# Performance work log

Measured on AMD Instinct MI355X. Metric: run time of the kernel, lower is better.

## Reference

```python
import jax, jax.numpy as jnp
import numpy as np


def _segment_sparsemax(x, batch, B):
    """Per-group sparsemax over a flat ragged tensor.

    x: [N] float values; batch: [N] sorted int group ids in [0, B).
    Groups are contiguous, so an in-group descending sort is a stable
    lexsort on (batch, -x); per-group cumsum is a global cumsum minus the
    cumsum value just before each group's start offset.
    """
    N = x.shape[0]
    num_nodes = jax.ops.segment_sum(jnp.ones(N, jnp.int32), batch, num_segments=B)  # [B]
    start = jnp.concatenate([jnp.zeros(1, jnp.int32), jnp.cumsum(num_nodes)[:-1]])  # [B]

    # shift by per-group max for numerical stability (as in torch forward)
    gmax = jax.ops.segment_max(x, batch, num_segments=B)
    xs = x - gmax[batch]

    # descending sort within each contiguous group
    order = jnp.lexsort((-xs, batch))
    sx = xs[order]  # [N], group-wise descending; group layout unchanged

    # per-group cumulative sum via global cumsum + start offsets
    cs = jnp.cumsum(sx)
    off = jnp.where(start > 0, cs[jnp.maximum(start - 1, 0)], jnp.zeros((), sx.dtype))  # [B]
    seg_cs = cs - off[batch] - 1.0  # input_cumsum - 1.0

    # rho = 1..n_g within each group
    rho = (jnp.arange(N, dtype=jnp.int32) - start[batch] + 1).astype(xs.dtype)

    support = rho * sx > seg_cs  # [N] bool
    supp_size = jax.ops.segment_sum(support.astype(jnp.int32), batch, num_segments=B)  # [B]

    idx = jnp.maximum(supp_size + start - 1, 0)  # [B]
    tau = seg_cs[idx] / supp_size.astype(xs.dtype)  # [B]

    return jnp.maximum(xs - tau[batch], 0.0)


def setup_inputs() -> dict:
    key = jax.random.key(0)
    k1, k2 = jax.random.split(key)
    N = 8_388_608
    B = 4096
    x = jax.random.normal(k1, (N,), dtype=jnp.float32)
    batch = jnp.sort(jax.random.randint(k2, (N,), 0, B)).astype(jnp.int64)
    return {"x": x, "batch": batch, "num_groups": B}


def reference(x, batch, num_groups):
    batch = batch.astype(jnp.int32)
    return _segment_sparsemax(x, batch, int(num_groups))
```

## Files before the change

kernel.cpp:

```cpp
#include <hip/hip_runtime.h>

#define BLK 256
#define QPT 3
#define CAPB (QPT * BLK * 4)
#define CCAP 320


__device__ __forceinline__ float wave_max(float v) {
#pragma unroll
  for (int o = 32; o; o >>= 1) v = fmaxf(v, __shfl_xor(v, o));
  return v;
}
__device__ __forceinline__ float wave_sum(float v) {
#pragma unroll
  for (int o = 32; o; o >>= 1) v += __shfl_xor(v, o);
  return v;
}
__device__ __forceinline__ int wave_sum_i(int v) {
#pragma unroll
  for (int o = 32; o; o >>= 1) v += __shfl_xor(v, o);
  return v;
}

__device__ __forceinline__ void block_sum_cnt(float& s, int& c, float* redf, int* redi, int tid) {
  s = wave_sum(s); c = wave_sum_i(c);
  __syncthreads();
  if ((tid & 63) == 0) { redf[tid >> 6] = s; redi[tid >> 6] = c; }
  __syncthreads();
  s = redf[0] + redf[1] + redf[2] + redf[3];
  c = redi[0] + redi[1] + redi[2] + redi[3];
}


extern "C" __global__ void __launch_bounds__(256)
build_starts(const int* __restrict__ batch, int* __restrict__ starts,
             const int* __restrict__ pB, int N) {
  const int B = *pB;
  const long long tid = (long long)blockIdx.x * 256 + threadIdx.x;
  const long long i0 = tid * 8;
  if (i0 >= N) return;
  int v[8];
  if (i0 + 8 <= N) {
    const int4 a = *(const int4*)(batch + i0);
    const int4 b = *(const int4*)(batch + i0 + 4);
    v[0] = a.x; v[1] = a.y; v[2] = a.z; v[3] = a.w;
    v[4] = b.x; v[5] = b.y; v[6] = b.z; v[7] = b.w;
  } else {
#pragma unroll
    for (int t = 0; t < 8; ++t) v[t] = (i0 + t < N) ? batch[i0 + t] : 0;
  }
  int prev = (i0 == 0) ? -1 : batch[i0 - 1];
#pragma unroll
  for (int t = 0; t < 8; ++t) {
    if (i0 + t >= N) break;
    const int cur = v[t];
    for (int g = prev + 1; g <= cur; ++g) starts[g] = (int)(i0 + t);
    prev = cur;
  }
  if (i0 + 8 >= N) {
    for (int g = prev + 1; g <= B; ++g) starts[g] = N;
  }
}


extern "C" __global__ void __launch_bounds__(BLK)
sparsemax_groups(const float* __restrict__ x, const int* __restrict__ starts,
                 const int* __restrict__ pB, float* __restrict__ out, int N) {
  __shared__ float redf[4];
  __shared__ int   redi[4];
  __shared__ float cand[CCAP];
  __shared__ float sorted[64];
  __shared__ int   s_cnt;
  __shared__ float s_csum;
  __shared__ float s_tau;
  const int tid  = threadIdx.x;
  const int lane = tid & 63;
  const int w    = tid >> 6;
  const int B = *pB;

  for (int g = blockIdx.x; g < B; g += gridDim.x) {
    const int s = starts[g];
    const int e = starts[g + 1];
    const int n = e - s;
    if (n <= 0) continue;
    const int a0 = s & ~3;

    if (e - a0 <= CAPB) {
      float4 r[QPT];
      float lmax = -INFINITY;
#pragma unroll
      for (int j = 0; j < QPT; ++j) {
        const int idx = a0 + (j * BLK + tid) * 4;
        float4 v = make_float4(-INFINITY, -INFINITY, -INFINITY, -INFINITY);
        if (idx < e) {
          if (idx + 4 <= N) {
            v = *(const float4*)(x + idx);
          } else {
            if (idx + 0 < N) v.x = x[idx + 0];
            if (idx + 1 < N) v.y = x[idx + 1];
            if (idx + 2 < N) v.z = x[idx + 2];
            if (idx + 3 < N) v.w = x[idx + 3];
          }
          if (idx + 0 < s || idx + 0 >= e) v.x = -INFINITY;
          if (idx + 1 < s || idx + 1 >= e) v.y = -INFINITY;
          if (idx + 2 < s || idx + 2 >= e) v.z = -INFINITY;
          if (idx + 3 < s || idx + 3 >= e) v.w = -INFINITY;
        }
        r[j] = v;
        lmax = fmaxf(lmax, fmaxf(fmaxf(v.x, v.y), fmaxf(v.z, v.w)));
      }
      lmax = wave_max(lmax);
      if (lane == 0) redf[w] = lmax;
      if (tid == 0) { s_cnt = 0; s_csum = 0.0f; }
      __syncthreads();
      const float gmax = fmaxf(fmaxf(redf[0], redf[1]), fmaxf(redf[2], redf[3]));
      const float thr = gmax - 1.0f;

      float wsum = 0.0f;
#pragma unroll
      for (int j = 0; j < QPT; ++j) {
        const float vv[4] = {r[j].x, r[j].y, r[j].z, r[j].w};
#pragma unroll
        for (int t = 0; t < 4; ++t) {
          const bool p = vv[t] > thr;
          const unsigned long long bal = __ballot(p);
          if (bal) {
            int base = 0;
            if (lane == 0) base = atomicAdd(&s_cnt, __popcll(bal));
            base = __shfl(base, 0);
            if (p) {
              const int off = base + __popcll(bal & ((1ull << lane) - 1ull));
              if (off < CCAP) cand[off] = vv[t];
              wsum += vv[t] - gmax;
            }
          }
        }
      }
      wsum = wave_sum(wsum);
      if (lane == 0) atomicAdd(&s_csum, wsum);
      __syncthreads();
      const int c = s_cnt;

      if (c <= 64) {
        if (w == 0) {
          const float v = (lane < c) ? cand[lane] - gmax : 0.0f;
          int rank = 0;
          for (int q = 0; q < c; ++q) {
            const float t = cand[q] - gmax;
            rank += (t > v) || (t == v && q < lane);
          }
          if (lane < c) sorted[rank] = v;
          const float sv = (lane < c) ? sorted[lane] : 0.0f;
          float cs = sv;
#pragma unroll
          for (int o = 1; o < 64; o <<= 1) {
            const float t2 = __shfl_up(cs, o);
            if (lane >= o) cs += t2;
          }
          const int flag = (lane < c) && (sv * (float)(lane + 1) > cs - 1.0f);
          const unsigned long long bal2 = __ballot(flag);
          const int k = 63 - __clzll(bal2);
          const float csk = __shfl(cs, k);
          if (lane == 0) s_tau = (csk - 1.0f) / (float)(k + 1);
        }
      } else if (c <= CCAP) {
        if (w == 0) {
          float tau = (s_csum - 1.0f) / (float)c;
          int cnt = c;
          for (int it = 0; it < 64; ++it) {
            float s2 = 0.0f; int c2 = 0;
            for (int q = lane; q < c; q += 64) {
              const float vs = cand[q] - gmax;
              if (vs > tau) { s2 += vs; c2++; }
            }
            s2 = wave_sum(s2); c2 = wave_sum_i(c2);
            if (c2 == cnt || c2 == 0) break;
            tau = (s2 - 1.0f) / (float)c2; cnt = c2;
          }
          if (lane == 0) s_tau = tau;
        }
      } else {
        float tau = (s_csum - 1.0f) / (float)c;
        int cnt = c;
        for (int it = 0; it < 64; ++it) {
          float s2 = 0.0f; int c2 = 0;
#pragma unroll
          for (int j = 0; j < QPT; ++j) {
            const float vv[4] = {r[j].x, r[j].y, r[j].z, r[j].w};
#pragma unroll
            for (int t = 0; t < 4; ++t) {
              const float vs = vv[t] - gmax;
              if (vs > tau) { s2 += vs; c2++; }
            }
          }
          block_sum_cnt(s2, c2, redf, redi, tid);
          if (c2 == cnt || c2 == 0) break;
          tau = (s2 - 1.0f) / (float)c2; cnt = c2;
        }
        if (tid == 0) s_tau = tau;
      }
      __syncthreads();
      const float sub = s_tau + gmax;

#pragma unroll
      for (int j = 0; j < QPT; ++j) {
        const int idx = a0 + (j * BLK + tid) * 4;
        if (idx >= e) continue;
        if (idx >= s && idx + 4 <= e) {
          float4 o4;
          o4.x = fmaxf(r[j].x - sub, 0.0f);
          o4.y = fmaxf(r[j].y - sub, 0.0f);
          o4.z = fmaxf(r[j].z - sub, 0.0f);
          o4.w = fmaxf(r[j].w - sub, 0.0f);
          *(float4*)(out + idx) = o4;
        } else {
          const float vv[4] = {r[j].x, r[j].y, r[j].z, r[j].w};
#pragma unroll
          for (int t = 0; t < 4; ++t) {
            const int p2 = idx + t;
            if (p2 >= s && p2 < e) out[p2] = fmaxf(vv[t] - sub, 0.0f);
          }
        }
      }
    } else {
      float gmax = -INFINITY;
      for (int i = s + tid; i < e; i += BLK) gmax = fmaxf(gmax, x[i]);
      gmax = wave_max(gmax);
      if (lane == 0) redf[w] = gmax;
      __syncthreads();
      gmax = fmaxf(fmaxf(redf[0], redf[1]), fmaxf(redf[2], redf[3]));
      float bs = 0.0f; int bc = 0;
      for (int i = s + tid; i < e; i += BLK) {
        const float vs = x[i] - gmax;
        if (vs > -1.0f) { bs += vs; bc++; }
      }
      block_sum_cnt(bs, bc, redf, redi, tid);
      float tau = (bs - 1.0f) / (float)bc;
      int cntS = bc;
      for (int it = 0; it < 64; ++it) {
        float s2 = 0.0f; int c2 = 0;
        for (int i = s + tid; i < e; i += BLK) {
          const float vs = x[i] - gmax;
          if (vs > tau) { s2 += vs; c2++; }
        }
        block_sum_cnt(s2, c2, redf, redi, tid);
        if (c2 == cntS || c2 == 0) break;
        tau = (s2 - 1.0f) / (float)c2; cntS = c2;
      }
      const float sub = tau + gmax;
      for (int i = s + tid; i < e; i += BLK) out[i] = fmaxf(x[i] - sub, 0.0f);
    }
  }
}

extern "C" void kernel_launch(void* const* d_in, const int* in_sizes, int n_in,
                              void* d_out, int out_size, void* d_ws, size_t ws_size,
                              hipStream_t stream) {
  const float* x     = (const float*)d_in[0];
  const int*   batch = (const int*)d_in[1];
  const int*   pB    = (const int*)d_in[2];
  float*       out   = (float*)d_out;
  const int N = in_sizes[0];

  int* starts = (int*)d_ws;

  const int g1 = (N + 2047) / 2048;
  build_starts<<<dim3(g1), dim3(256), 0, stream>>>(batch, starts, pB, N);
  sparsemax_groups<<<dim3(4096), dim3(BLK), 0, stream>>>(x, starts, pB, out, N);
}
```

Measured before the change: 111.7 us.

## Process one group per wavefront instead of one group per block

Each 64-lane wavefront now handles a whole group on its own: registers hold up to 10 float4 per lane, and candidate compaction uses a running wave-local count instead of LDS atomics. All block-level reductions and __syncthreads are replaced by wave shuffles, and each wave gets its own candidate and sort buffers. The grid shrinks to 1024 blocks of 4 waves, so there is still one wave per group. The goal is to remove block barriers and atomics, at the cost of higher register pressure and less parallelism within each group.

```diff
diff --git a/kernel.cpp b/kernel.cpp
--- a/kernel.cpp
+++ b/kernel.cpp
@@ -1,8 +1,8 @@
 #include <hip/hip_runtime.h>
 
 #define BLK 256
-#define QPT 3
-#define CAPB (QPT * BLK * 4)
+#define WPT 10
+#define WCAP (WPT * 64 * 4)
 #define CCAP 320
 
 
@@ -20,15 +20,6 @@
 #pragma unroll
   for (int o = 32; o; o >>= 1) v += __shfl_xor(v, o);
   return v;
-}
-
-__device__ __forceinline__ void block_sum_cnt(float& s, int& c, float* redf, int* redi, int tid) {
-  s = wave_sum(s); c = wave_sum_i(c);
-  __syncthreads();
-  if ((tid & 63) == 0) { redf[tid >> 6] = s; redi[tid >> 6] = c; }
-  __syncthreads();
-  s = redf[0] + redf[1] + redf[2] + redf[3];
-  c = redi[0] + redi[1] + redi[2] + redi[3];
 }
 
 
@@ -66,31 +57,26 @@
 extern "C" __global__ void __launch_bounds__(BLK)
 sparsemax_groups(const float* __restrict__ x, const int* __restrict__ starts,
                  const int* __restrict__ pB, float* __restrict__ out, int N) {
-  __shared__ float redf[4];
-  __shared__ int   redi[4];
-  __shared__ float cand[CCAP];
-  __shared__ float sorted[64];
-  __shared__ int   s_cnt;
-  __shared__ float s_csum;
-  __shared__ float s_tau;
+  __shared__ float cand[4][CCAP];
+  __shared__ float sorted_[4][64];
   const int tid  = threadIdx.x;
   const int lane = tid & 63;
   const int w    = tid >> 6;
   const int B = *pB;
 
-  for (int g = blockIdx.x; g < B; g += gridDim.x) {
+  for (int g = blockIdx.x * 4 + w; g < B; g += gridDim.x * 4) {
     const int s = starts[g];
     const int e = starts[g + 1];
     const int n = e - s;
     if (n <= 0) continue;
     const int a0 = s & ~3;
 
-    if (e - a0 <= CAPB) {
-      float4 r[QPT];
+    if (e - a0 <= WCAP) {
+      float4 r[WPT];
       float lmax = -INFINITY;
 #pragma unroll
-      for (int j = 0; j < QPT; ++j) {
-        const int idx = a0 + (j * BLK + tid) * 4;
+      for (int j = 0; j < WPT; ++j) {
+        const int idx = a0 + (j * 64 + lane) * 4;
         float4 v = make_float4(-INFINITY, -INFINITY, -INFINITY, -INFINITY);
         if (idx < e) {
           if (idx + 4 <= N) {
@@ -109,83 +95,72 @@
         r[j] = v;
         lmax = fmaxf(lmax, fmaxf(fmaxf(v.x, v.y), fmaxf(v.z, v.w)));
       }
-      lmax = wave_max(lmax);
-      if (lane == 0) redf[w] = lmax;
-      if (tid == 0) { s_cnt = 0; s_csum = 0.0f; }
-      __syncthreads();
-      const float gmax = fmaxf(fmaxf(redf[0], redf[1]), fmaxf(redf[2], redf[3]));
+      const float gmax = wave_max(lmax);
       const float thr = gmax - 1.0f;
 
+      int cnt = 0;
       float wsum = 0.0f;
 #pragma unroll
-      for (int j = 0; j < QPT; ++j) {
+      for (int j = 0; j < WPT; ++j) {
         const float vv[4] = {r[j].x, r[j].y, r[j].z, r[j].w};
 #pragma unroll
         for (int t = 0; t < 4; ++t) {
           const bool p = vv[t] > thr;
           const unsigned long long bal = __ballot(p);
           if (bal) {
-            int base = 0;
-            if (lane == 0) base = atomicAdd(&s_cnt, __popcll(bal));
-            base = __shfl(base, 0);
             if (p) {
-              const int off = base + __popcll(bal & ((1ull << lane) - 1ull));
-              if (off < CCAP) cand[off] = vv[t];
+              const int off = cnt + __popcll(bal & ((1ull << lane) - 1ull));
+              if (off < CCAP) cand[w][off] = vv[t];
               wsum += vv[t] - gmax;
             }
+            cnt += __popcll(bal);
           }
         }
       }
       wsum = wave_sum(wsum);
-      if (lane == 0) atomicAdd(&s_csum, wsum);
-      __syncthreads();
-      const int c = s_cnt;
-
+      const int c = cnt;
+
+      float tau;
       if (c <= 64) {
-        if (w == 0) {
-          const float v = (lane < c) ? cand[lane] - gmax : 0.0f;
-          int rank = 0;
-          for (int q = 0; q < c; ++q) {
-            const float t = cand[q] - gmax;
-            rank += (t > v) || (t == v && q < lane);
-          }
-          if (lane < c) sorted[rank] = v;
-          const float sv = (lane < c) ? sorted[lane] : 0.0f;
-          float cs = sv;
-#pragma unroll
-          for (int o = 1; o < 64; o <<= 1) {
-            const float t2 = __shfl_up(cs, o);
-            if (lane >= o) cs += t2;
-          }
-          const int flag = (lane < c) && (sv * (float)(lane + 1) > cs - 1.0f);
-          const unsigned long long bal2 = __ballot(flag);
-          const int k = 63 - __clzll(bal2);
-          const float csk = __shfl(cs, k);
-          if (lane == 0) s_tau = (csk - 1.0f) / (float)(k + 1);
-        }
+        const float v = (lane < c) ? cand[w][lane] - gmax : 0.0f;
+        int rank = 0;
+        for (int q = 0; q < c; ++q) {
+          const float t = cand[w][q] - gmax;
+          rank += (t > v) || (t == v && q < lane);
+        }
+        if (lane < c) sorted_[w][rank] = v;
+        const float sv = (lane < c) ? sorted_[w][lane] : 0.0f;
+        float cs = sv;
+#pragma unroll
+        for (int o = 1; o < 64; o <<= 1) {
+          const float t2 = __shfl_up(cs, o);
+          if (lane >= o) cs += t2;
+        }
+        const int flag = (lane < c) && (sv * (float)(lane + 1) > cs - 1.0f);
+        const unsigned long long bal2 = __ballot(flag);
+        const int k = 63 - __clzll(bal2);
+        const float csk = __shfl(cs, k);
+        tau = (csk - 1.0f) / (float)(k + 1);
       } else if (c <= CCAP) {
-        if (w == 0) {
-          float tau = (s_csum - 1.0f) / (float)c;
-          int cnt = c;
-          for (int it = 0; it < 64; ++it) {
-            float s2 = 0.0f; int c2 = 0;
-            for (int q = lane; q < c; q += 64) {
-              const float vs = cand[q] - gmax;
-              if (vs > tau) { s2 += vs; c2++; }
-            }
-            s2 = wave_sum(s2); c2 = wave_sum_i(c2);
-            if (c2 == cnt || c2 == 0) break;
-            tau = (s2 - 1.0f) / (float)c2; cnt = c2;
-          }
-          if (lane == 0) s_tau = tau;
-        }
-      } else {
-        float tau = (s_csum - 1.0f) / (float)c;
-        int cnt = c;
+        tau = (wsum - 1.0f) / (float)c;
+        int cnt2 = c;
         for (int it = 0; it < 64; ++it) {
           float s2 = 0.0f; int c2 = 0;
-#pragma unroll
-          for (int j = 0; j < QPT; ++j) {
+          for (int q = lane; q < c; q += 64) {
+            const float vs = cand[w][q] - gmax;
+            if (vs > tau) { s2 += vs; c2++; }
+          }
+          s2 = wave_sum(s2); c2 = wave_sum_i(c2);
+          if (c2 == cnt2 || c2 == 0) break;
+          tau = (s2 - 1.0f) / (float)c2; cnt2 = c2;
+        }
+      } else {
+        tau = (wsum - 1.0f) / (float)c;
+        int cnt2 = c;
+        for (int it = 0; it < 64; ++it) {
+          float s2 = 0.0f; int c2 = 0;
+#pragma unroll
+          for (int j = 0; j < WPT; ++j) {
             const float vv[4] = {r[j].x, r[j].y, r[j].z, r[j].w};
 #pragma unroll
             for (int t = 0; t < 4; ++t) {
@@ -193,18 +168,17 @@
               if (vs > tau) { s2 += vs; c2++; }
             }
           }
-          block_sum_cnt(s2, c2, redf, redi, tid);
-          if (c2 == cnt || c2 == 0) break;
-          tau = (s2 - 1.0f) / (float)c2; cnt = c2;
-        }
-        if (tid == 0) s_tau = tau;
-      }
-      __syncthreads();
-      const float sub = s_tau + gmax;
-
-#pragma unroll
-      for (int j = 0; j < QPT; ++j) {
-        const int idx = a0 + (j * BLK + tid) * 4;
+          s2 = wave_sum(s2); c2 = wave_sum_i(c2);
+          if (c2 == cnt2 || c2 == 0) break;
+          tau = (s2 - 1.0f) / (float)c2; cnt2 = c2;
+        }
+      }
+
+      const float sub = tau + gmax;
+
+#pragma unroll
+      for (int j = 0; j < WPT; ++j) {
+        const int idx = a0 + (j * 64 + lane) * 4;
         if (idx >= e) continue;
         if (idx >= s && idx + 4 <= e) {
           float4 o4;
@@ -224,31 +198,28 @@
       }
     } else {
       float gmax = -INFINITY;
-      for (int i = s + tid; i < e; i += BLK) gmax = fmaxf(gmax, x[i]);
+      for (int i = s + lane; i < e; i += 64) gmax = fmaxf(gmax, x[i]);
       gmax = wave_max(gmax);
-      if (lane == 0) redf[w] = gmax;
-      __syncthreads();
-      gmax = fmaxf(fmaxf(redf[0], redf[1]), fmaxf(redf[2], redf[3]));
       float bs = 0.0f; int bc = 0;
-      for (int i = s + tid; i < e; i += BLK) {
+      for (int i = s + lane; i < e; i += 64) {
         const float vs = x[i] - gmax;
         if (vs > -1.0f) { bs += vs; bc++; }
       }
-      block_sum_cnt(bs, bc, redf, redi, tid);
+      bs = wave_sum(bs); bc = wave_sum_i(bc);
       float tau = (bs - 1.0f) / (float)bc;
       int cntS = bc;
       for (int it = 0; it < 64; ++it) {
         float s2 = 0.0f; int c2 = 0;
-        for (int i = s + tid; i < e; i += BLK) {
+        for (int i = s + lane; i < e; i += 64) {
           const float vs = x[i] - gmax;
           if (vs > tau) { s2 += vs; c2++; }
         }
-        block_sum_cnt(s2, c2, redf, redi, tid);
+        s2 = wave_sum(s2); c2 = wave_sum_i(c2);
         if (c2 == cntS || c2 == 0) break;
         tau = (s2 - 1.0f) / (float)c2; cntS = c2;
       }
       const float sub = tau + gmax;
-      for (int i = s + tid; i < e; i += BLK) out[i] = fmaxf(x[i] - sub, 0.0f);
+      for (int i = s + lane; i < e; i += 64) out[i] = fmaxf(x[i] - sub, 0.0f);
     }
   }
 }
@@ -266,5 +237,5 @@
 
   const int g1 = (N + 2047) / 2048;
   build_starts<<<dim3(g1), dim3(256), 0, stream>>>(batch, starts, pB, N);
-  sparsemax_groups<<<dim3(4096), dim3(BLK), 0, stream>>>(x, starts, pB, out, N);
-}
+  sparsemax_groups<<<dim3(1024), dim3(BLK), 0, stream>>>(x, starts, pB, out, N);
+}
```

New measurement: 113.4 us. No clear change (+1.5%).
